# Optimization experiments

Hardware: AMD Instinct MI355X
Metric: run time of the kernel (lower is better)

## Reference

```python
import jax, jax.numpy as jnp
import numpy as np

B, T, I, H, C = 4096, 512, 1, 32, 2


def setup_inputs() -> dict:
    key = jax.random.key(0)
    ks = jax.random.split(key, 7)
    k_ih = 1.0 / np.sqrt(H)  # PyTorch GRU init bound (uniform, but normal*scale is fine for a numeric reference)
    x = jax.random.normal(ks[0], (B, T, I), dtype=jnp.float32)
    W_ih = jax.random.normal(ks[1], (3 * H, I), dtype=jnp.float32) * k_ih
    W_hh = jax.random.normal(ks[2], (3 * H, H), dtype=jnp.float32) * k_ih
    b_ih = jax.random.normal(ks[3], (3 * H,), dtype=jnp.float32) * k_ih
    b_hh = jax.random.normal(ks[4], (3 * H,), dtype=jnp.float32) * k_ih
    fc_w = jax.random.normal(ks[5], (C, H), dtype=jnp.float32) * k_ih
    fc_b = jax.random.normal(ks[6], (C,), dtype=jnp.float32) * k_ih
    return {"x": x, "W_ih": W_ih, "W_hh": W_hh, "b_ih": b_ih, "b_hh": b_hh, "fc_w": fc_w, "fc_b": fc_b}


def _gru_last_hidden(x, W_ih, W_hh, b_ih, b_hh):
    # Precompute input projections for all timesteps: [B, T, 3H]
    xg = jnp.einsum('bti,gi->btg', x, W_ih) + b_ih
    xg_t = jnp.swapaxes(xg, 0, 1)  # [T, B, 3H] for scan over time
    h0 = jnp.zeros((x.shape[0], W_hh.shape[1]), dtype=x.dtype)

    def step(h, xg_step):
        hg = h @ W_hh.T + b_hh  # [B, 3H]
        xr, xz, xn = jnp.split(xg_step, 3, axis=-1)
        hr, hz, hn = jnp.split(hg, 3, axis=-1)
        r = jax.nn.sigmoid(xr + hr)
        z = jax.nn.sigmoid(xz + hz)
        n = jnp.tanh(xn + r * hn)
        h_new = (1.0 - z) * n + z * h  # PyTorch GRU update rule
        return h_new, None

    hT, _ = jax.lax.scan(step, h0, xg_t)
    return hT  # [B, H] == out[:, -1, :]


def reference(x, W_ih, W_hh, b_ih, b_hh, fc_w, fc_b):
    hT = _gru_last_hidden(x, W_ih, W_hh, b_ih, b_hh)
    return hT @ fc_w.T + fc_b  # [B, C]
```

## Files before the change

### kernel.cpp

```cpp
#include <hip/hip_runtime.h>
#include <hip/hip_bf16.h>


typedef _Float16 half2v __attribute__((ext_vector_type(2)));

__device__ __forceinline__ float fdot2f(int a, int b, float c) {
    return __builtin_amdgcn_fdot2(__builtin_bit_cast(half2v, a),
                                  __builtin_bit_cast(half2v, b), c, false);
}

__device__ __forceinline__ int pkf16(float lo, float hi) {
    return __builtin_bit_cast(int, __builtin_amdgcn_cvt_pkrtz(lo, hi));
}

__device__ __forceinline__ float sigm(float a) {
    float e = __builtin_amdgcn_exp2f(a * -1.442695041f);
    return __builtin_amdgcn_rcpf(1.0f + e);
}

#define FOR16(M) M(0) M(1) M(2) M(3) M(4) M(5) M(6) M(7) \
                 M(8) M(9) M(10) M(11) M(12) M(13) M(14) M(15)

__global__ __launch_bounds__(256, 1)
void gru_fused_kernel(const float* __restrict__ x,
                      const float* __restrict__ W_ih,
                      const float* __restrict__ W_hh,
                      const float* __restrict__ b_ih,
                      const float* __restrict__ b_hh,
                      const float* __restrict__ fc_w,
                      const float* __restrict__ fc_b,
                      float* __restrict__ out)
{
    const int tid = threadIdx.x;
    const int j   = tid & 31;
    const int g   = tid >> 5;
    const int bb  = blockIdx.x * 8 + g;

    __shared__ float xs[8 * 516];
    __shared__ unsigned short hbuf[8][32];

    {
        const float* xbase = x + (size_t)blockIdx.x * 8 * 512;
        #pragma unroll
        for (int k = 0; k < 16; ++k) {
            int idx = tid + k * 256;
            int b   = idx >> 9, p = idx & 511;
            xs[b * 516 + p] = xbase[idx];
        }
    }

#define DECLW(p) int wr##p, wz##p, wn##p;
    FOR16(DECLW)
#undef DECLW

    {
        const float4* wrp = reinterpret_cast<const float4*>(W_hh + (j) * 32);
        const float4* wzp = reinterpret_cast<const float4*>(W_hh + (32 + j) * 32);
        const float4* wnp = reinterpret_cast<const float4*>(W_hh + (64 + j) * 32);
#define INITQ(q, p0, p1)                                \
        {                                               \
            float4 a = wrp[q], b = wzp[q], c = wnp[q];  \
            wr##p0 = pkf16(a.x, a.y);                   \
            wr##p1 = pkf16(a.z, a.w);                   \
            wz##p0 = pkf16(b.x, b.y);                   \
            wz##p1 = pkf16(b.z, b.w);                   \
            wn##p0 = pkf16(c.x, c.y);                   \
            wn##p1 = pkf16(c.z, c.w);                   \
        }
        INITQ(0, 0, 1)  INITQ(1, 2, 3)  INITQ(2, 4, 5)  INITQ(3, 6, 7)
        INITQ(4, 8, 9)  INITQ(5, 10, 11) INITQ(6, 12, 13) INITQ(7, 14, 15)
#undef INITQ
    }

    const float br   = b_ih[j]      + b_hh[j];
    const float bz   = b_ih[32 + j] + b_hh[32 + j];
    const float bin  = b_ih[64 + j];
    const float bhn  = b_hh[64 + j];
    const float wihr = W_ih[j];
    const float wihz = W_ih[32 + j];
    const float wihn = W_ih[64 + j];

    float h = 0.0f;
    hbuf[g][j] = 0;
    __syncthreads();

    for (int c = 0; c < 16; ++c) {
        const float* xc = &xs[g * 516 + c * 32];

        #pragma unroll
        for (int tt = 0; tt < 32; ++tt) {
            float xb = xc[tt];

            const int4* hp = reinterpret_cast<const int4*>(&hbuf[g][0]);
            int4 A = hp[0], B = hp[1], C = hp[2], D = hp[3];

            float ar = fmaf(xb, wihr, br);
            float az = fmaf(xb, wihz, bz);
            float an = bhn;
            ar = fdot2f(wr0,  A.x, ar); az = fdot2f(wz0,  A.x, az); an = fdot2f(wn0,  A.x, an);
            ar = fdot2f(wr1,  A.y, ar); az = fdot2f(wz1,  A.y, az); an = fdot2f(wn1,  A.y, an);
            ar = fdot2f(wr2,  A.z, ar); az = fdot2f(wz2,  A.z, az); an = fdot2f(wn2,  A.z, an);
            ar = fdot2f(wr3,  A.w, ar); az = fdot2f(wz3,  A.w, az); an = fdot2f(wn3,  A.w, an);
            ar = fdot2f(wr4,  B.x, ar); az = fdot2f(wz4,  B.x, az); an = fdot2f(wn4,  B.x, an);
            ar = fdot2f(wr5,  B.y, ar); az = fdot2f(wz5,  B.y, az); an = fdot2f(wn5,  B.y, an);
            ar = fdot2f(wr6,  B.z, ar); az = fdot2f(wz6,  B.z, az); an = fdot2f(wn6,  B.z, an);
            ar = fdot2f(wr7,  B.w, ar); az = fdot2f(wz7,  B.w, az); an = fdot2f(wn7,  B.w, an);
            ar = fdot2f(wr8,  C.x, ar); az = fdot2f(wz8,  C.x, az); an = fdot2f(wn8,  C.x, an);
            ar = fdot2f(wr9,  C.y, ar); az = fdot2f(wz9,  C.y, az); an = fdot2f(wn9,  C.y, an);
            ar = fdot2f(wr10, C.z, ar); az = fdot2f(wz10, C.z, az); an = fdot2f(wn10, C.z, an);
            ar = fdot2f(wr11, C.w, ar); az = fdot2f(wz11, C.w, az); an = fdot2f(wn11, C.w, an);
            ar = fdot2f(wr12, D.x, ar); az = fdot2f(wz12, D.x, az); an = fdot2f(wn12, D.x, an);
            ar = fdot2f(wr13, D.y, ar); az = fdot2f(wz13, D.y, az); an = fdot2f(wn13, D.y, an);
            ar = fdot2f(wr14, D.z, ar); az = fdot2f(wz14, D.z, az); an = fdot2f(wn14, D.z, an);
            ar = fdot2f(wr15, D.w, ar); az = fdot2f(wz15, D.w, az); an = fdot2f(wn15, D.w, an);

            float r = sigm(ar);
            float z = sigm(az);
            float npre = fmaf(r, an, fmaf(xb, wihn, bin));
            float e2 = __builtin_amdgcn_exp2f(npre * 2.885390082f);
            float t  = __builtin_amdgcn_rcpf(1.0f + e2);
            float n  = fmaf(-2.0f, t, 1.0f);
            h = fmaf(z, h - n, n);

            hbuf[g][j] = __builtin_bit_cast(unsigned short, (_Float16)h);
        }
    }

    float s0 = h * fc_w[j];
    float s1 = h * fc_w[32 + j];
    #pragma unroll
    for (int off = 16; off >= 1; off >>= 1) {
        s0 += __shfl_xor(s0, off, 32);
        s1 += __shfl_xor(s1, off, 32);
    }
    if (j == 0) {
        out[(size_t)bb * 2 + 0] = s0 + fc_b[0];
        out[(size_t)bb * 2 + 1] = s1 + fc_b[1];
    }
}

extern "C" void kernel_launch(void* const* d_in, const int* in_sizes, int n_in,
                              void* d_out, int out_size, void* d_ws, size_t ws_size,
                              hipStream_t stream)
{
    const float* x    = (const float*)d_in[0];
    const float* W_ih = (const float*)d_in[1];
    const float* W_hh = (const float*)d_in[2];
    const float* b_ih = (const float*)d_in[3];
    const float* b_hh = (const float*)d_in[4];
    const float* fc_w = (const float*)d_in[5];
    const float* fc_b = (const float*)d_in[6];
    float* out = (float*)d_out;

    dim3 grid(512), block(256);
    hipLaunchKernelGGL(gru_fused_kernel, grid, block, 0, stream,
                       x, W_ih, W_hh, b_ih, b_hh, fc_w, fc_b, out);
}
```

Baseline: 167.0 us.

## Process two batch sequences per thread to interleave independent recurrences

```diff
diff --git a/kernel.cpp b/kernel.cpp
--- a/kernel.cpp
+++ b/kernel.cpp
@@ -34,15 +34,16 @@
     const int tid = threadIdx.x;
     const int j   = tid & 31;
     const int g   = tid >> 5;
-    const int bb  = blockIdx.x * 8 + g;
+    const int b0  = 2 * g;
+    const int b1  = 2 * g + 1;
 
-    __shared__ float xs[8 * 516];
-    __shared__ unsigned short hbuf[8][32];
+    __shared__ float xs[16 * 516];
+    __shared__ unsigned short hbuf[16][32];
 
     {
-        const float* xbase = x + (size_t)blockIdx.x * 8 * 512;
+        const float* xbase = x + (size_t)blockIdx.x * 16 * 512;
         #pragma unroll
-        for (int k = 0; k < 16; ++k) {
+        for (int k = 0; k < 32; ++k) {
             int idx = tid + k * 256;
             int b   = idx >> 9, p = idx & 511;
             xs[b * 516 + p] = xbase[idx];
@@ -80,62 +81,79 @@
     const float wihz = W_ih[32 + j];
     const float wihn = W_ih[64 + j];
 
-    float h = 0.0f;
-    hbuf[g][j] = 0;
+    float h0 = 0.0f, h1 = 0.0f;
+    hbuf[b0][j] = 0;
+    hbuf[b1][j] = 0;
     __syncthreads();
 
+    const float* xc0 = &xs[b0 * 516];
+    const float* xc1 = &xs[b1 * 516];
+
     for (int c = 0; c < 16; ++c) {
-        const float* xc = &xs[g * 516 + c * 32];
+        #pragma unroll 8
+        for (int tt = 0; tt < 32; ++tt) {
+            const int t = c * 32 + tt;
+            float xb0 = xc0[t];
+            float xb1 = xc1[t];
 
-        #pragma unroll
-        for (int tt = 0; tt < 32; ++tt) {
-            float xb = xc[tt];
+            const int4* hp0 = reinterpret_cast<const int4*>(&hbuf[b0][0]);
+            const int4* hp1 = reinterpret_cast<const int4*>(&hbuf[b1][0]);
+            int4 A0 = hp0[0], B0 = hp0[1], C0 = hp0[2], D0 = hp0[3];
+            int4 A1 = hp1[0], B1 = hp1[1], C1 = hp1[2], D1 = hp1[3];
 
-            const int4* hp = reinterpret_cast<const int4*>(&hbuf[g][0]);
-            int4 A = hp[0], B = hp[1], C = hp[2], D = hp[3];
+            float ar0 = fmaf(xb0, wihr, br), ar1 = fmaf(xb1, wihr, br);
+            float az0 = fmaf(xb0, wihz, bz), az1 = fmaf(xb1, wihz, bz);
+            float an0 = bhn,                 an1 = bhn;
 
-            float ar = fmaf(xb, wihr, br);
-            float az = fmaf(xb, wihz, bz);
-            float an = bhn;
-            ar = fdot2f(wr0,  A.x, ar); az = fdot2f(wz0,  A.x, az); an = fdot2f(wn0,  A.x, an);
-            ar = fdot2f(wr1,  A.y, ar); az = fdot2f(wz1,  A.y, az); an = fdot2f(wn1,  A.y, an);
-            ar = fdot2f(wr2,  A.z, ar); az = fdot2f(wz2,  A.z, az); an = fdot2f(wn2,  A.z, an);
-            ar = fdot2f(wr3,  A.w, ar); az = fdot2f(wz3,  A.w, az); an = fdot2f(wn3,  A.w, an);
-            ar = fdot2f(wr4,  B.x, ar); az = fdot2f(wz4,  B.x, az); an = fdot2f(wn4,  B.x, an);
-            ar = fdot2f(wr5,  B.y, ar); az = fdot2f(wz5,  B.y, az); an = fdot2f(wn5,  B.y, an);
-            ar = fdot2f(wr6,  B.z, ar); az = fdot2f(wz6,  B.z, az); an = fdot2f(wn6,  B.z, an);
-            ar = fdot2f(wr7,  B.w, ar); az = fdot2f(wz7,  B.w, az); an = fdot2f(wn7,  B.w, an);
-            ar = fdot2f(wr8,  C.x, ar); az = fdot2f(wz8,  C.x, az); an = fdot2f(wn8,  C.x, an);
-            ar = fdot2f(wr9,  C.y, ar); az = fdot2f(wz9,  C.y, az); an = fdot2f(wn9,  C.y, an);
-            ar = fdot2f(wr10, C.z, ar); az = fdot2f(wz10, C.z, az); an = fdot2f(wn10, C.z, an);
-            ar = fdot2f(wr11, C.w, ar); az = fdot2f(wz11, C.w, az); an = fdot2f(wn11, C.w, an);
-            ar = fdot2f(wr12, D.x, ar); az = fdot2f(wz12, D.x, az); an = fdot2f(wn12, D.x, an);
-            ar = fdot2f(wr13, D.y, ar); az = fdot2f(wz13, D.y, az); an = fdot2f(wn13, D.y, an);
-            ar = fdot2f(wr14, D.z, ar); az = fdot2f(wz14, D.z, az); an = fdot2f(wn14, D.z, an);
-            ar = fdot2f(wr15, D.w, ar); az = fdot2f(wz15, D.w, az); an = fdot2f(wn15, D.w, an);
+#define D2(P, HK0, HK1)                                            \
+            ar0 = fdot2f(wr##P, HK0, ar0); ar1 = fdot2f(wr##P, HK1, ar1); \
+            az0 = fdot2f(wz##P, HK0, az0); az1 = fdot2f(wz##P, HK1, az1); \
+            an0 = fdot2f(wn##P, HK0, an0); an1 = fdot2f(wn##P, HK1, an1);
+            D2(0,  A0.x, A1.x)  D2(1,  A0.y, A1.y)
+            D2(2,  A0.z, A1.z)  D2(3,  A0.w, A1.w)
+            D2(4,  B0.x, B1.x)  D2(5,  B0.y, B1.y)
+            D2(6,  B0.z, B1.z)  D2(7,  B0.w, B1.w)
+            D2(8,  C0.x, C1.x)  D2(9,  C0.y, C1.y)
+            D2(10, C0.z, C1.z)  D2(11, C0.w, C1.w)
+            D2(12, D0.x, D1.x)  D2(13, D0.y, D1.y)
+            D2(14, D0.z, D1.z)  D2(15, D0.w, D1.w)
+#undef D2
 
-            float r = sigm(ar);
-            float z = sigm(az);
-            float npre = fmaf(r, an, fmaf(xb, wihn, bin));
-            float e2 = __builtin_amdgcn_exp2f(npre * 2.885390082f);
-            float t  = __builtin_amdgcn_rcpf(1.0f + e2);
-            float n  = fmaf(-2.0f, t, 1.0f);
-            h = fmaf(z, h - n, n);
+            float r0 = sigm(ar0), r1 = sigm(ar1);
+            float z0 = sigm(az0), z1 = sigm(az1);
+            float np0 = fmaf(r0, an0, fmaf(xb0, wihn, bin));
+            float np1 = fmaf(r1, an1, fmaf(xb1, wihn, bin));
+            float e0 = __builtin_amdgcn_exp2f(np0 * 2.885390082f);
+            float e1 = __builtin_amdgcn_exp2f(np1 * 2.885390082f);
+            float t0 = __builtin_amdgcn_rcpf(1.0f + e0);
+            float t1 = __builtin_amdgcn_rcpf(1.0f + e1);
+            float n0 = fmaf(-2.0f, t0, 1.0f);
+            float n1 = fmaf(-2.0f, t1, 1.0f);
+            h0 = fmaf(z0, h0 - n0, n0);
+            h1 = fmaf(z1, h1 - n1, n1);
 
-            hbuf[g][j] = __builtin_bit_cast(unsigned short, (_Float16)h);
+            hbuf[b0][j] = __builtin_bit_cast(unsigned short, (_Float16)h0);
+            hbuf[b1][j] = __builtin_bit_cast(unsigned short, (_Float16)h1);
         }
     }
 
-    float s0 = h * fc_w[j];
-    float s1 = h * fc_w[32 + j];
+    const float f0 = fc_w[j], f1 = fc_w[32 + j];
+    float s00 = h0 * f0, s01 = h0 * f1;
+    float s10 = h1 * f0, s11 = h1 * f1;
     #pragma unroll
     for (int off = 16; off >= 1; off >>= 1) {
-        s0 += __shfl_xor(s0, off, 32);
-        s1 += __shfl_xor(s1, off, 32);
+        s00 += __shfl_xor(s00, off, 32);
+        s01 += __shfl_xor(s01, off, 32);
+        s10 += __shfl_xor(s10, off, 32);
+        s11 += __shfl_xor(s11, off, 32);
     }
     if (j == 0) {
-        out[(size_t)bb * 2 + 0] = s0 + fc_b[0];
-        out[(size_t)bb * 2 + 1] = s1 + fc_b[1];
+        const size_t gb0 = (size_t)blockIdx.x * 16 + b0;
+        const size_t gb1 = (size_t)blockIdx.x * 16 + b1;
+        out[gb0 * 2 + 0] = s00 + fc_b[0];
+        out[gb0 * 2 + 1] = s01 + fc_b[1];
+        out[gb1 * 2 + 0] = s10 + fc_b[0];
+        out[gb1 * 2 + 1] = s11 + fc_b[1];
     }
 }
 
@@ -152,7 +170,7 @@
     const float* fc_b = (const float*)d_in[6];
     float* out = (float*)d_out;
 
-    dim3 grid(512), block(256);
+    dim3 grid(256), block(256);
     hipLaunchKernelGGL(gru_fused_kernel, grid, block, 0, stream,
                        x, W_ih, W_hh, b_ih, b_hh, fc_w, fc_b, out);
 }
```

New measurement: 170.7 us. 1.02x slower.
